# Performance work log

Hardware: AMD Instinct MI355X
Metric: run time of the kernel (lower is better)

The kernel has to match this reference:

```python
import jax, jax.numpy as jnp
import numpy as np

E = 1024
H = 16
D = E // H
T = 1024
S = 1024
B = 8
MASK_FILL = 1e-30  # note: module fills masked scores with 1e-30, NOT -inf


def setup_inputs() -> dict:
    key = jax.random.key(0)
    ks = jax.random.split(key, 8)
    inp = {
        "query1": jax.random.normal(ks[0], (T, B, E), jnp.float32),
        "query2": jax.random.normal(ks[1], (T, B, E), jnp.float32),
        "key": jax.random.normal(ks[2], (S, B, E), jnp.float32),
        "value": jax.random.normal(ks[3], (S, B, E), jnp.float32),
        # causal mask: True = masked
        "attn_mask": jnp.triu(jnp.ones((T, S), jnp.bool_), k=1),
        # xavier-uniform-ish weights (torch stores Linear weight as [out, in])
        "q_w": jax.random.uniform(ks[4], (E, E), jnp.float32, -1, 1) * np.sqrt(6.0 / (2 * E)),
        "k_w": jax.random.uniform(ks[5], (E, E), jnp.float32, -1, 1) * np.sqrt(6.0 / (2 * E)),
        "v_w": jax.random.uniform(ks[6], (E, E), jnp.float32, -1, 1) * np.sqrt(6.0 / (2 * E)),
        "out_w": jax.random.uniform(ks[7], (E, E), jnp.float32, -1, 1) * np.sqrt(6.0 / (2 * E)),
    }
    return inp


def _split_heads(x):
    # [L, B, E] -> [B, H, L, D]
    L = x.shape[0]
    return x.reshape(L, B, H, D).transpose(1, 2, 0, 3)


def reference(query1, query2, key, value, attn_mask, q_w, k_w, v_w, out_w):
    scaling = float(D) ** -0.5
    q1 = _split_heads(query1 @ q_w.T) * scaling  # [B,H,T,D]
    q2 = _split_heads(query2 @ q_w.T) * scaling
    k = _split_heads(key @ k_w.T)                # [B,H,S,D]
    v = _split_heads(value @ v_w.T)

    # ---- stream s (second query stream attends first) ----
    scores_s = jnp.einsum("bhtd,bhsd->bhts", q2, k)
    scores_s = jnp.where(attn_mask[None, None], MASK_FILL, scores_s)
    probs_s = jax.nn.softmax(scores_s, axis=-1)
    o_s = jnp.einsum("bhts,bhsd->bhtd", probs_s, v)  # [B,H,T,D]

    # k/v update between passes (requires T == S)
    k2 = k + o_s
    v2 = v + o_s

    # ---- stream d ----
    scores_d = jnp.einsum("bhtd,bhsd->bhts", q1, k2)
    scores_d = jnp.where(attn_mask[None, None], MASK_FILL, scores_d)
    probs_d = jax.nn.softmax(scores_d, axis=-1)
    o_d = jnp.einsum("bhts,bhsd->bhtd", probs_d, v2)

    def _merge_and_proj(o):
        # [B,H,T,D] -> [T,B,E] -> out proj (no bias)
        return o.transpose(2, 0, 1, 3).reshape(T, B, E) @ out_w.T

    attn_output_s = _merge_and_proj(o_s)
    attn_output_d = _merge_and_proj(o_d)
    attn_s = probs_s.mean(axis=1)  # [B,T,S]
    attn_d = probs_d.mean(axis=1)
    return attn_output_d, attn_d, attn_output_s, attn_s
```

## Files before the change

kernel.cpp:

```cpp
#include <hip/hip_runtime.h>
#include <cstddef>

#define T_DIM 1024
#define S_DIM 1024
#define B_DIM 8
#define E_DIM 1024
#define H_DIM 16
#define D_DIM 64
#define NBHTD (B_DIM*H_DIM*T_DIM*D_DIM)

typedef __attribute__((ext_vector_type(8))) short short8;
typedef __attribute__((ext_vector_type(4))) float floatx4;

__device__ inline unsigned short f2bf(float x){
    union { float f; unsigned u; } v; v.f = x;
    unsigned r = (v.u + 0x7FFFu + ((v.u >> 16) & 1u)) >> 16;
    return (unsigned short)r;
}
__device__ inline float bf2f(unsigned short h){
    union { float f; unsigned u; } v; v.u = ((unsigned)h) << 16; return v.f;
}

typedef __attribute__((address_space(1))) const unsigned int* gptr_t;
typedef __attribute__((address_space(3))) unsigned int* lptr_t;
__device__ inline void gl_lds16(const void* g, void* l){
    __builtin_amdgcn_global_load_lds((gptr_t)g, (lptr_t)l, 16, 0, 0);
}

__device__ inline int swz(int row, int s){
    int ch = (s >> 2) ^ (row & 7);
    return (row << 10) + (ch << 2) + (s & 3);
}

__global__ __launch_bounds__(256)
void split_pair(const float* __restrict__ src, unsigned short* __restrict__ hi,
                unsigned short* __restrict__ lo, float scale)
{
    size_t i = ((size_t)blockIdx.x*256 + threadIdx.x)*8;
    float4 a = *(const float4*)(src+i);
    float4 b = *(const float4*)(src+i+4);
    float v[8] = {a.x,a.y,a.z,a.w,b.x,b.y,b.z,b.w};
    short8 h8, l8;
    #pragma unroll
    for (int j = 0; j < 8; ++j) {
        float x = v[j]*scale;
        unsigned short hh = f2bf(x);
        h8[j] = (short)hh;
        l8[j] = (short)f2bf(x - bf2f(hh));
    }
    *(short8*)(hi+i) = h8;
    *(short8*)(lo+i) = l8;
}

template <int AMODE, int CMODE>
__global__ __launch_bounds__(256, 2)
void gemm_bf3(const unsigned short* __restrict__ Ahi, const unsigned short* __restrict__ Alo,
              const unsigned short* __restrict__ Bhi, const unsigned short* __restrict__ Blo,
              float* __restrict__ Cf,
              unsigned short* __restrict__ Chi, unsigned short* __restrict__ Clo)
{
    __shared__ __align__(16) unsigned short lds[4][128*32];

    const int tid  = threadIdx.x;
    const int n0   = blockIdx.x * 128;
    const int m0   = blockIdx.y * 128;
    const int wave = tid >> 6, lane = tid & 63;
    const int lrow = lane & 15, quad = lane >> 4;
    const int mw = (wave & 1)*64, nw = (wave >> 1)*64;

    floatx4 acc[4][4];
    #pragma unroll
    for (int i = 0; i < 4; ++i)
        #pragma unroll
        for (int j = 0; j < 4; ++j) acc[i][j] = (floatx4){0.f,0.f,0.f,0.f};

    for (int kk = 0; kk < 1024; kk += 32) {
        __syncthreads();
        #pragma unroll
        for (int rnd = 0; rnd < 2; ++rnd) {
            int c = rnd*256 + tid;
            int row = c >> 2, col8 = (c & 3)*8;
            size_t aoff;
            if (AMODE == 0) {
                aoff = (size_t)(m0+row)*1024 + kk + col8;
            } else {
                int r = m0 + row; int t = r >> 3, bb = r & 7;
                int h = kk >> 6, d0 = (kk & 63) + col8;
                aoff = (((size_t)(bb*H_DIM + h)*T_DIM) + t)*D_DIM + d0;
            }
            size_t boff = (size_t)(n0+row)*1024 + kk + col8;
            gl_lds16(Ahi + aoff, &lds[0][c*8]);
            gl_lds16(Alo + aoff, &lds[1][c*8]);
            gl_lds16(Bhi + boff, &lds[2][c*8]);
            gl_lds16(Blo + boff, &lds[3][c*8]);
        }
        __syncthreads();

        short8 ah[4], al[4], bh[4], bl[4];
        #pragma unroll
        for (int mt = 0; mt < 4; ++mt) {
            int r = mw + mt*16 + lrow;
            ah[mt] = *(const short8*)&lds[0][r*32 + quad*8];
            al[mt] = *(const short8*)&lds[1][r*32 + quad*8];
        }
        #pragma unroll
        for (int nt = 0; nt < 4; ++nt) {
            int r = nw + nt*16 + lrow;
            bh[nt] = *(const short8*)&lds[2][r*32 + quad*8];
            bl[nt] = *(const short8*)&lds[3][r*32 + quad*8];
        }
        #pragma unroll
        for (int mt = 0; mt < 4; ++mt)
            #pragma unroll
            for (int nt = 0; nt < 4; ++nt) {
                acc[mt][nt] = __builtin_amdgcn_mfma_f32_16x16x32_bf16(ah[mt], bh[nt], acc[mt][nt], 0,0,0);
                acc[mt][nt] = __builtin_amdgcn_mfma_f32_16x16x32_bf16(ah[mt], bl[nt], acc[mt][nt], 0,0,0);
                acc[mt][nt] = __builtin_amdgcn_mfma_f32_16x16x32_bf16(al[mt], bh[nt], acc[mt][nt], 0,0,0);
            }
    }

    #pragma unroll
    for (int mt = 0; mt < 4; ++mt) {
        #pragma unroll
        for (int nt = 0; nt < 4; ++nt) {
            int n = n0 + nw + nt*16 + lrow;
            #pragma unroll
            for (int r = 0; r < 4; ++r) {
                int m = m0 + mw + mt*16 + quad*4 + r;
                float v = acc[mt][nt][r];
                if (CMODE == 2) {
                    Cf[(size_t)m*1024 + n] = v;
                } else {
                    int t = m >> 3, bb = m & 7;
                    int h = n >> 6, d = n & 63;
                    size_t idx = (((size_t)(bb*H_DIM + h)*T_DIM) + t)*D_DIM + d;
                    if (CMODE == 0) {
                        Cf[idx] = v;
                    } else {
                        unsigned short hh = f2bf(v);
                        Chi[idx] = hh;
                        Clo[idx] = f2bf(v - bf2f(hh));
                    }
                }
            }
        }
    }
}

__global__ __launch_bounds__(256)
void split_vt(const float* __restrict__ Vh, unsigned short* __restrict__ Vthi,
              unsigned short* __restrict__ Vtlo)
{
    __shared__ float tile[64][68];
    const int bh = blockIdx.y, s0 = blockIdx.x*64;
    const int tid = threadIdx.x;
    const size_t base = (size_t)bh*S_DIM*D_DIM;

    {
        int r = tid >> 2, c0 = (tid & 3) * 16;
        const float* p = Vh + base + (size_t)(s0 + r)*D_DIM + c0;
        float4 a = *(const float4*)p;
        float4 b = *(const float4*)(p+4);
        float4 c = *(const float4*)(p+8);
        float4 d = *(const float4*)(p+12);
        *(float4*)&tile[r][c0]    = a;
        *(float4*)&tile[r][c0+4]  = b;
        *(float4*)&tile[r][c0+8]  = c;
        *(float4*)&tile[r][c0+12] = d;
    }
    __syncthreads();
    {
        int d = tid >> 2, cs = (tid & 3) * 16;
        short8 hi[2], lo[2];
        #pragma unroll
        for (int half = 0; half < 2; ++half)
            #pragma unroll
            for (int u = 0; u < 8; ++u) {
                float x = tile[cs + half*8 + u][d];
                unsigned short hh = f2bf(x);
                hi[half][u] = (short)hh;
                lo[half][u] = (short)f2bf(x - bf2f(hh));
            }
        size_t obase = base + (size_t)d*S_DIM + s0 + cs;
        *(short8*)(Vthi + obase)     = hi[0];
        *(short8*)(Vthi + obase + 8) = hi[1];
        *(short8*)(Vtlo + obase)     = lo[0];
        *(short8*)(Vtlo + obase + 8) = lo[1];
    }
}

__global__ __launch_bounds__(256, 2)
void attn_mfma(const float* __restrict__ Qh,
               const unsigned short* __restrict__ Khi, const unsigned short* __restrict__ Klo,
               const unsigned short* __restrict__ Vthi, const unsigned short* __restrict__ Vtlo,
               float* __restrict__ Ofp,
               unsigned short* __restrict__ Ohi, unsigned short* __restrict__ Olo,
               float* __restrict__ attn_mean)
{
    const int b  = blockIdx.y;
    const int t0 = blockIdx.x * 16;
    const int tid  = threadIdx.x;
    const int lane = tid & 63;
    const int wave = tid >> 6;
    const int lrow = lane & 15;
    const int quad = lane >> 4;

    __shared__ float sc[16 * 1024];

    float accm[4][16];
    #pragma unroll
    for (int j = 0; j < 4; ++j)
        #pragma unroll
        for (int c = 0; c < 16; ++c) accm[j][c] = 0.f;

    #pragma unroll 1
    for (int h = 0; h < H_DIM; ++h) {
        const int bh = b*H_DIM + h;
        const size_t kbase = (size_t)bh * S_DIM * D_DIM;

        short8 qh0, ql0, qh1, ql1;
        {
            const float* qp = Qh + kbase + (size_t)(t0 + lrow)*D_DIM + quad*8;
            float4 a  = *(const float4*)qp;
            float4 b4 = *(const float4*)(qp+4);
            float4 c4 = *(const float4*)(qp+32);
            float4 d4 = *(const float4*)(qp+36);
            float va[8] = {a.x,a.y,a.z,a.w,b4.x,b4.y,b4.z,b4.w};
            float vb8[8] = {c4.x,c4.y,c4.z,c4.w,d4.x,d4.y,d4.z,d4.w};
            #pragma unroll
            for (int j = 0; j < 8; ++j) {
                unsigned short h0 = f2bf(va[j]);
                qh0[j] = (short)h0; ql0[j] = (short)f2bf(va[j] - bf2f(h0));
                unsigned short h1 = f2bf(vb8[j]);
                qh1[j] = (short)h1; ql1[j] = (short)f2bf(vb8[j] - bf2f(h1));
            }
        }

        __syncthreads();

        #pragma unroll 1
        for (int jt = 0; jt < 16; ++jt) {
            const int s0 = wave*256 + jt*16;
            const unsigned short* kp_h = Khi + kbase + (size_t)(s0 + lrow)*D_DIM + quad*8;
            const unsigned short* kp_l = Klo + kbase + (size_t)(s0 + lrow)*D_DIM + quad*8;
            short8 kh0 = *(const short8*)(kp_h);
            short8 kh1 = *(const short8*)(kp_h + 32);
            short8 kl0 = *(const short8*)(kp_l);
            short8 kl1 = *(const short8*)(kp_l + 32);
            floatx4 acc = {0.f,0.f,0.f,0.f};
            acc = __builtin_amdgcn_mfma_f32_16x16x32_bf16(qh0, kh0, acc, 0,0,0);
            acc = __builtin_amdgcn_mfma_f32_16x16x32_bf16(qh1, kh1, acc, 0,0,0);
            acc = __builtin_amdgcn_mfma_f32_16x16x32_bf16(qh0, kl0, acc, 0,0,0);
            acc = __builtin_amdgcn_mfma_f32_16x16x32_bf16(qh1, kl1, acc, 0,0,0);
            acc = __builtin_amdgcn_mfma_f32_16x16x32_bf16(ql0, kh0, acc, 0,0,0);
            acc = __builtin_amdgcn_mfma_f32_16x16x32_bf16(ql1, kh1, acc, 0,0,0);
            const int s_g = s0 + lrow;
            #pragma unroll
            for (int r = 0; r < 4; ++r) {
                int q = quad*4 + r;
                float v = (s_g > t0 + q) ? 1e-30f : acc[r];
                sc[swz(q, s_g)] = v;
            }
        }
        __syncthreads();

        #pragma unroll 1
        for (int j = 0; j < 4; ++j) {
            const int row = wave*4 + j;
            float2 vb[8];
            float m = -3.0e38f;
            #pragma unroll
            for (int c = 0; c < 8; ++c) {
                int s = lane*2 + 128*c;
                vb[c] = *(const float2*)&sc[swz(row, s)];
                m = fmaxf(m, fmaxf(vb[c].x, vb[c].y));
            }
            #pragma unroll
            for (int off = 32; off > 0; off >>= 1) m = fmaxf(m, __shfl_xor(m, off));
            float sum = 0.f;
            #pragma unroll
            for (int c = 0; c < 8; ++c) {
                vb[c].x = __expf(vb[c].x - m);
                vb[c].y = __expf(vb[c].y - m);
                sum += vb[c].x + vb[c].y;
            }
            #pragma unroll
            for (int off = 32; off > 0; off >>= 1) sum += __shfl_xor(sum, off);
            const float inv = 1.0f / sum;
            #pragma unroll
            for (int c = 0; c < 8; ++c) {
                int s = lane*2 + 128*c;
                float p0 = vb[c].x * inv, p1 = vb[c].y * inv;
                accm[j][2*c]   += p0;
                accm[j][2*c+1] += p1;
                float2 pw; pw.x = p0; pw.y = p1;
                *(float2*)&sc[swz(row, s)] = pw;
            }
        }
        __syncthreads();

        {
            const int d0 = wave*16;
            const unsigned short* vh = Vthi + kbase + (size_t)(d0 + lrow)*S_DIM;
            const unsigned short* vl = Vtlo + kbase + (size_t)(d0 + lrow)*S_DIM;
            floatx4 oa = {0.f,0.f,0.f,0.f}, ob = {0.f,0.f,0.f,0.f};
            #pragma unroll 2
            for (int sk = 0; sk < S_DIM; sk += 32) {
                const int sa = sk + quad*8;
                float4 p0 = *(const float4*)&sc[swz(lrow, sa)];
                float4 p1 = *(const float4*)&sc[swz(lrow, sa+4)];
                short8 af;
                af[0]=(short)f2bf(p0.x); af[1]=(short)f2bf(p0.y);
                af[2]=(short)f2bf(p0.z); af[3]=(short)f2bf(p0.w);
                af[4]=(short)f2bf(p1.x); af[5]=(short)f2bf(p1.y);
                af[6]=(short)f2bf(p1.z); af[7]=(short)f2bf(p1.w);
                short8 bh8 = *(const short8*)(vh + sa);
                short8 bl8 = *(const short8*)(vl + sa);
                oa = __builtin_amdgcn_mfma_f32_16x16x32_bf16(af, bh8, oa, 0,0,0);
                ob = __builtin_amdgcn_mfma_f32_16x16x32_bf16(af, bl8, ob, 0,0,0);
            }
            #pragma unroll
            for (int r = 0; r < 4; ++r) {
                int q = quad*4 + r;
                float v = oa[r] + ob[r];
                size_t idx = kbase + (size_t)(t0+q)*D_DIM + d0 + lrow;
                if (Ofp) Ofp[idx] = v;
                unsigned short hh = f2bf(v);
                Ohi[idx] = hh;
                Olo[idx] = f2bf(v - bf2f(hh));
            }
        }
    }

    #pragma unroll
    for (int j = 0; j < 4; ++j) {
        int row = wave*4 + j;
        #pragma unroll
        for (int c = 0; c < 8; ++c) {
            float2 p;
            p.x = accm[j][2*c]   * (1.0f/H_DIM);
            p.y = accm[j][2*c+1] * (1.0f/H_DIM);
            *(float2*)&attn_mean[((size_t)b*T_DIM + t0 + row)*S_DIM + lane*2 + 128*c] = p;
        }
    }
}

__global__ __launch_bounds__(256)
void add_k(unsigned short* __restrict__ Khi, unsigned short* __restrict__ Klo,
           const float* __restrict__ O)
{
    size_t i = ((size_t)blockIdx.x*256 + threadIdx.x)*8;
    short8 hi = *(short8*)(Khi+i), lo = *(short8*)(Klo+i);
    float4 o0 = *(const float4*)(O+i), o1 = *(const float4*)(O+i+4);
    float ov[8] = {o0.x,o0.y,o0.z,o0.w,o1.x,o1.y,o1.z,o1.w};
    short8 nh, nl;
    #pragma unroll
    for (int j = 0; j < 8; ++j) {
        float k = bf2f((unsigned short)hi[j]) + bf2f((unsigned short)lo[j]) + ov[j];
        unsigned short hh = f2bf(k);
        nh[j] = (short)hh;
        nl[j] = (short)f2bf(k - bf2f(hh));
    }
    *(short8*)(Khi+i) = nh;
    *(short8*)(Klo+i) = nl;
}

__global__ __launch_bounds__(256)
void add_v(float* __restrict__ V, const float* __restrict__ O)
{
    size_t i = ((size_t)blockIdx.x*256 + threadIdx.x)*4;
    float4 o = *(const float4*)(O+i);
    float4 v = *(const float4*)(V+i);
    v.x+=o.x; v.y+=o.y; v.z+=o.z; v.w+=o.w;
    *(float4*)(V+i) = v;
}

extern "C" void kernel_launch(void* const* d_in, const int* in_sizes, int n_in,
                              void* d_out, int out_size, void* d_ws, size_t ws_size,
                              hipStream_t stream)
{
    const float* q1  = (const float*)d_in[0];
    const float* q2  = (const float*)d_in[1];
    const float* key = (const float*)d_in[2];
    const float* val = (const float*)d_in[3];
    const float* qw  = (const float*)d_in[5];
    const float* kw  = (const float*)d_in[6];
    const float* vw  = (const float*)d_in[7];
    const float* ow  = (const float*)d_in[8];

    float* out   = (float*)d_out;
    float* outd  = out;
    float* attnd = out + 1*(size_t)NBHTD;
    float* outs  = out + 2*(size_t)NBHTD;
    float* attns = out + 3*(size_t)NBHTD;

    unsigned short* ws_u16 = (unsigned short*)d_ws;
    unsigned short* Khi  = ws_u16;
    unsigned short* Klo  = Khi  + (size_t)NBHTD;
    unsigned short* Vthi = Klo  + (size_t)NBHTD;
    unsigned short* Vtlo = Vthi + (size_t)NBHTD;
    unsigned short* R2a  = Vtlo + (size_t)NBHTD;
    unsigned short* R2b  = R2a  + 2*(size_t)NBHTD;

    const size_t EE = (size_t)E_DIM*E_DIM;
    unsigned short* qwhi = R2a;
    unsigned short* qwlo = qwhi + EE;
    unsigned short* kwhi = qwlo + EE;
    unsigned short* kwlo = kwhi + EE;
    unsigned short* vwhi = kwlo + EE;
    unsigned short* vwlo = vwhi + EE;
    float* Osb = (float*)R2a;
    unsigned short* Odhi = R2a;
    unsigned short* Odlo = Odhi + (size_t)NBHTD;
    unsigned short* Oshi = R2b;
    unsigned short* Oslo = Oshi + (size_t)NBHTD;
    unsigned short* owhi = ws_u16;
    unsigned short* owlo = owhi + EE;

    float* Q1h = outd;
    float* Q2h = outs;
    float* Vh  = attnd;
    unsigned short* Ahi = (unsigned short*)attns;
    unsigned short* Alo = Ahi + (size_t)NBHTD;

    const dim3 ggrid(8, 64);

    split_pair<<<512, 256, 0, stream>>>(qw, qwhi, qwlo, 1.f);
    split_pair<<<512, 256, 0, stream>>>(kw, kwhi, kwlo, 1.f);
    split_pair<<<512, 256, 0, stream>>>(vw, vwhi, vwlo, 1.f);

    split_pair<<<4096, 256, 0, stream>>>(key, Ahi, Alo, 1.f);
    gemm_bf3<0,1><<<ggrid, 256, 0, stream>>>(Ahi, Alo, kwhi, kwlo, nullptr, Khi, Klo);

    split_pair<<<4096, 256, 0, stream>>>(val, Ahi, Alo, 1.f);
    gemm_bf3<0,0><<<ggrid, 256, 0, stream>>>(Ahi, Alo, vwhi, vwlo, Vh, nullptr, nullptr);
    split_vt<<<dim3(16, 128), 256, 0, stream>>>(Vh, Vthi, Vtlo);

    split_pair<<<4096, 256, 0, stream>>>(q1, Ahi, Alo, 0.125f);
    gemm_bf3<0,0><<<ggrid, 256, 0, stream>>>(Ahi, Alo, qwhi, qwlo, Q1h, nullptr, nullptr);

    split_pair<<<4096, 256, 0, stream>>>(q2, Ahi, Alo, 0.125f);
    gemm_bf3<0,0><<<ggrid, 256, 0, stream>>>(Ahi, Alo, qwhi, qwlo, Q2h, nullptr, nullptr);

    attn_mfma<<<dim3(64, 8), 256, 0, stream>>>(Q2h, Khi, Klo, Vthi, Vtlo,
                                               Osb, Oshi, Oslo, attns);

    add_k<<<4096, 256, 0, stream>>>(Khi, Klo, Osb);
    add_v<<<8192, 256, 0, stream>>>(Vh, Osb);
    split_vt<<<dim3(16, 128), 256, 0, stream>>>(Vh, Vthi, Vtlo);

    attn_mfma<<<dim3(64, 8), 256, 0, stream>>>(Q1h, Khi, Klo, Vthi, Vtlo,
                                               nullptr, Odhi, Odlo, attnd);

    split_pair<<<512, 256, 0, stream>>>(ow, owhi, owlo, 1.f);
    gemm_bf3<1,2><<<ggrid, 256, 0, stream>>>(Oshi, Oslo, owhi, owlo, outs, nullptr, nullptr);
    gemm_bf3<1,2><<<ggrid, 256, 0, stream>>>(Odhi, Odlo, owhi, owlo, outd, nullptr, nullptr);
}
```

Baseline: 1.895 ms.

## Keep attention scores in registers with split softmax and bf16 P in LDS

The attention kernel now swaps the MFMA operand order so each lane holds a column of scores in registers. Softmax runs in registers, and only per-wave max and sum pairs are exchanged through LDS, instead of writing fp32 scores to LDS and reading them back. Probabilities are converted to bf16 once and stored in a smaller swizzled LDS buffer, which the PV stage reads directly. The change also software-prefetches K tiles, remaps the grid so adjacent blocks span batches, and widens the attn_mean stores to float4. The cost is much higher register pressure (sv, accm, mt arrays), which may cause spills or lower occupancy.

```diff
diff --git a/kernel.cpp b/kernel.cpp
--- a/kernel.cpp
+++ b/kernel.cpp
@@ -10,6 +10,7 @@
 #define NBHTD (B_DIM*H_DIM*T_DIM*D_DIM)
 
 typedef __attribute__((ext_vector_type(8))) short short8;
+typedef __attribute__((ext_vector_type(4))) short short4v;
 typedef __attribute__((ext_vector_type(4))) float floatx4;
 
 __device__ inline unsigned short f2bf(float x){
@@ -27,9 +28,8 @@
     __builtin_amdgcn_global_load_lds((gptr_t)g, (lptr_t)l, 16, 0, 0);
 }
 
-__device__ inline int swz(int row, int s){
-    int ch = (s >> 2) ^ (row & 7);
-    return (row << 10) + (ch << 2) + (s & 3);
+__device__ inline int poff(int row, int s){
+    return (row << 10) + ((((s >> 3) ^ (row & 7)) << 3)) + (s & 7);
 }
 
 __global__ __launch_bounds__(256)
@@ -197,21 +197,22 @@
                unsigned short* __restrict__ Ohi, unsigned short* __restrict__ Olo,
                float* __restrict__ attn_mean)
 {
-    const int b  = blockIdx.y;
-    const int t0 = blockIdx.x * 16;
+    const int bid = blockIdx.x;
+    const int b   = bid & 7;
+    const int t0  = (bid >> 3) * 16;
     const int tid  = threadIdx.x;
     const int lane = tid & 63;
     const int wave = tid >> 6;
     const int lrow = lane & 15;
     const int quad = lane >> 4;
-
-    __shared__ float sc[16 * 1024];
-
-    float accm[4][16];
+    const int t_g  = t0 + lrow;
+
+    __shared__ __align__(16) unsigned short plds[16*1024];
+    __shared__ float2 stats[4][16];
+
+    float accm[64];
     #pragma unroll
-    for (int j = 0; j < 4; ++j)
-        #pragma unroll
-        for (int c = 0; c < 16; ++c) accm[j][c] = 0.f;
+    for (int i = 0; i < 64; ++i) accm[i] = 0.f;
 
     #pragma unroll 1
     for (int h = 0; h < H_DIM; ++h) {
@@ -225,7 +226,7 @@
             float4 b4 = *(const float4*)(qp+4);
             float4 c4 = *(const float4*)(qp+32);
             float4 d4 = *(const float4*)(qp+36);
-            float va[8] = {a.x,a.y,a.z,a.w,b4.x,b4.y,b4.z,b4.w};
+            float va[8]  = {a.x,a.y,a.z,a.w,b4.x,b4.y,b4.z,b4.w};
             float vb8[8] = {c4.x,c4.y,c4.z,c4.w,d4.x,d4.y,d4.z,d4.w};
             #pragma unroll
             for (int j = 0; j < 8; ++j) {
@@ -236,66 +237,85 @@
             }
         }
 
+        float sv[64];
+        {
+            const unsigned short* kph = Khi + kbase + (size_t)(wave*256 + lrow)*D_DIM + quad*8;
+            const unsigned short* kpl = Klo + kbase + (size_t)(wave*256 + lrow)*D_DIM + quad*8;
+            short8 kh0 = *(const short8*)(kph);
+            short8 kh1 = *(const short8*)(kph + 32);
+            short8 kl0 = *(const short8*)(kpl);
+            short8 kl1 = *(const short8*)(kpl + 32);
+            #pragma unroll
+            for (int jt = 0; jt < 16; ++jt) {
+                short8 nh0, nh1, nl0, nl1;
+                if (jt < 15) {
+                    const unsigned short* nph = kph + (jt+1)*16*D_DIM;
+                    const unsigned short* npl = kpl + (jt+1)*16*D_DIM;
+                    nh0 = *(const short8*)(nph);
+                    nh1 = *(const short8*)(nph + 32);
+                    nl0 = *(const short8*)(npl);
+                    nl1 = *(const short8*)(npl + 32);
+                }
+                floatx4 acc = {0.f,0.f,0.f,0.f};
+                acc = __builtin_amdgcn_mfma_f32_16x16x32_bf16(kh0, qh0, acc, 0,0,0);
+                acc = __builtin_amdgcn_mfma_f32_16x16x32_bf16(kh1, qh1, acc, 0,0,0);
+                acc = __builtin_amdgcn_mfma_f32_16x16x32_bf16(kl0, qh0, acc, 0,0,0);
+                acc = __builtin_amdgcn_mfma_f32_16x16x32_bf16(kl1, qh1, acc, 0,0,0);
+                acc = __builtin_amdgcn_mfma_f32_16x16x32_bf16(kh0, ql0, acc, 0,0,0);
+                acc = __builtin_amdgcn_mfma_f32_16x16x32_bf16(kh1, ql1, acc, 0,0,0);
+                const int sb = wave*256 + jt*16 + quad*4;
+                #pragma unroll
+                for (int r = 0; r < 4; ++r)
+                    sv[jt*4+r] = (sb + r > t_g) ? 1e-30f : acc[r];
+                kh0 = nh0; kh1 = nh1; kl0 = nl0; kl1 = nl1;
+            }
+        }
+
+        float mt[32];
+        #pragma unroll
+        for (int i = 0; i < 32; ++i) mt[i] = fmaxf(sv[i], sv[i+32]);
+        #pragma unroll
+        for (int st = 16; st > 0; st >>= 1) {
+            #pragma unroll
+            for (int i = 0; i < st; ++i) mt[i] = fmaxf(mt[i], mt[i+st]);
+        }
+        float m_loc = fmaxf(mt[0], __shfl_xor(mt[0], 16));
+        m_loc = fmaxf(m_loc, __shfl_xor(m_loc, 32));
+
+        #pragma unroll
+        for (int i = 0; i < 64; ++i) sv[i] = __expf(sv[i] - m_loc);
+        float st2[32];
+        #pragma unroll
+        for (int i = 0; i < 32; ++i) st2[i] = sv[i] + sv[i+32];
+        #pragma unroll
+        for (int st = 16; st > 0; st >>= 1) {
+            #pragma unroll
+            for (int i = 0; i < st; ++i) st2[i] += st2[i+st];
+        }
+        float s_loc = st2[0] + __shfl_xor(st2[0], 16);
+        s_loc += __shfl_xor(s_loc, 32);
+
+        if (quad == 0) stats[wave][lrow] = make_float2(m_loc, s_loc);
         __syncthreads();
 
-        #pragma unroll 1
+        float2 c0 = stats[0][lrow], c1 = stats[1][lrow];
+        float2 c2 = stats[2][lrow], c3 = stats[3][lrow];
+        float m_g = fmaxf(fmaxf(c0.x, c1.x), fmaxf(c2.x, c3.x));
+        float sum_g = c0.y*__expf(c0.x - m_g) + c1.y*__expf(c1.x - m_g)
+                    + c2.y*__expf(c2.x - m_g) + c3.y*__expf(c3.x - m_g);
+        const float myscale = __expf(m_loc - m_g) / sum_g;
+
+        #pragma unroll
         for (int jt = 0; jt < 16; ++jt) {
-            const int s0 = wave*256 + jt*16;
-            const unsigned short* kp_h = Khi + kbase + (size_t)(s0 + lrow)*D_DIM + quad*8;
-            const unsigned short* kp_l = Klo + kbase + (size_t)(s0 + lrow)*D_DIM + quad*8;
-            short8 kh0 = *(const short8*)(kp_h);
-            short8 kh1 = *(const short8*)(kp_h + 32);
-            short8 kl0 = *(const short8*)(kp_l);
-            short8 kl1 = *(const short8*)(kp_l + 32);
-            floatx4 acc = {0.f,0.f,0.f,0.f};
-            acc = __builtin_amdgcn_mfma_f32_16x16x32_bf16(qh0, kh0, acc, 0,0,0);
-            acc = __builtin_amdgcn_mfma_f32_16x16x32_bf16(qh1, kh1, acc, 0,0,0);
-            acc = __builtin_amdgcn_mfma_f32_16x16x32_bf16(qh0, kl0, acc, 0,0,0);
-            acc = __builtin_amdgcn_mfma_f32_16x16x32_bf16(qh1, kl1, acc, 0,0,0);
-            acc = __builtin_amdgcn_mfma_f32_16x16x32_bf16(ql0, kh0, acc, 0,0,0);
-            acc = __builtin_amdgcn_mfma_f32_16x16x32_bf16(ql1, kh1, acc, 0,0,0);
-            const int s_g = s0 + lrow;
-            #pragma unroll
-            for (int r = 0; r < 4; ++r) {
-                int q = quad*4 + r;
-                float v = (s_g > t0 + q) ? 1e-30f : acc[r];
-                sc[swz(q, s_g)] = v;
-            }
-        }
-        __syncthreads();
-
-        #pragma unroll 1
-        for (int j = 0; j < 4; ++j) {
-            const int row = wave*4 + j;
-            float2 vb[8];
-            float m = -3.0e38f;
-            #pragma unroll
-            for (int c = 0; c < 8; ++c) {
-                int s = lane*2 + 128*c;
-                vb[c] = *(const float2*)&sc[swz(row, s)];
-                m = fmaxf(m, fmaxf(vb[c].x, vb[c].y));
-            }
-            #pragma unroll
-            for (int off = 32; off > 0; off >>= 1) m = fmaxf(m, __shfl_xor(m, off));
-            float sum = 0.f;
-            #pragma unroll
-            for (int c = 0; c < 8; ++c) {
-                vb[c].x = __expf(vb[c].x - m);
-                vb[c].y = __expf(vb[c].y - m);
-                sum += vb[c].x + vb[c].y;
-            }
-            #pragma unroll
-            for (int off = 32; off > 0; off >>= 1) sum += __shfl_xor(sum, off);
-            const float inv = 1.0f / sum;
-            #pragma unroll
-            for (int c = 0; c < 8; ++c) {
-                int s = lane*2 + 128*c;
-                float p0 = vb[c].x * inv, p1 = vb[c].y * inv;
-                accm[j][2*c]   += p0;
-                accm[j][2*c+1] += p1;
-                float2 pw; pw.x = p0; pw.y = p1;
-                *(float2*)&sc[swz(row, s)] = pw;
-            }
+            float p0 = sv[jt*4+0]*myscale, p1 = sv[jt*4+1]*myscale;
+            float p2 = sv[jt*4+2]*myscale, p3 = sv[jt*4+3]*myscale;
+            accm[jt*4+0] += p0; accm[jt*4+1] += p1;
+            accm[jt*4+2] += p2; accm[jt*4+3] += p3;
+            short4v pk;
+            pk[0] = (short)f2bf(p0); pk[1] = (short)f2bf(p1);
+            pk[2] = (short)f2bf(p2); pk[3] = (short)f2bf(p3);
+            const int sidx = wave*256 + jt*16 + quad*4;
+            *(short4v*)&plds[poff(lrow, sidx)] = pk;
         }
         __syncthreads();
 
@@ -304,16 +324,10 @@
             const unsigned short* vh = Vthi + kbase + (size_t)(d0 + lrow)*S_DIM;
             const unsigned short* vl = Vtlo + kbase + (size_t)(d0 + lrow)*S_DIM;
             floatx4 oa = {0.f,0.f,0.f,0.f}, ob = {0.f,0.f,0.f,0.f};
-            #pragma unroll 2
+            #pragma unroll 4
             for (int sk = 0; sk < S_DIM; sk += 32) {
                 const int sa = sk + quad*8;
-                float4 p0 = *(const float4*)&sc[swz(lrow, sa)];
-                float4 p1 = *(const float4*)&sc[swz(lrow, sa+4)];
-                short8 af;
-                af[0]=(short)f2bf(p0.x); af[1]=(short)f2bf(p0.y);
-                af[2]=(short)f2bf(p0.z); af[3]=(short)f2bf(p0.w);
-                af[4]=(short)f2bf(p1.x); af[5]=(short)f2bf(p1.y);
-                af[6]=(short)f2bf(p1.z); af[7]=(short)f2bf(p1.w);
+                short8 af  = *(const short8*)&plds[poff(lrow, sa)];
                 short8 bh8 = *(const short8*)(vh + sa);
                 short8 bl8 = *(const short8*)(vl + sa);
                 oa = __builtin_amdgcn_mfma_f32_16x16x32_bf16(af, bh8, oa, 0,0,0);
@@ -332,15 +346,16 @@
         }
     }
 
-    #pragma unroll
-    for (int j = 0; j < 4; ++j) {
-        int row = wave*4 + j;
-        #pragma unroll
-        for (int c = 0; c < 8; ++c) {
-            float2 p;
-            p.x = accm[j][2*c]   * (1.0f/H_DIM);
-            p.y = accm[j][2*c+1] * (1.0f/H_DIM);
-            *(float2*)&attn_mean[((size_t)b*T_DIM + t0 + row)*S_DIM + lane*2 + 128*c] = p;
+    {
+        float* am = attn_mean + ((size_t)b*T_DIM + t_g)*S_DIM + wave*256 + quad*4;
+        #pragma unroll
+        for (int jt = 0; jt < 16; ++jt) {
+            float4 p4;
+            p4.x = accm[jt*4+0]*(1.0f/H_DIM);
+            p4.y = accm[jt*4+1]*(1.0f/H_DIM);
+            p4.z = accm[jt*4+2]*(1.0f/H_DIM);
+            p4.w = accm[jt*4+3]*(1.0f/H_DIM);
+            *(float4*)(am + jt*16) = p4;
         }
     }
 }
@@ -442,15 +457,15 @@
     split_pair<<<4096, 256, 0, stream>>>(q2, Ahi, Alo, 0.125f);
     gemm_bf3<0,0><<<ggrid, 256, 0, stream>>>(Ahi, Alo, qwhi, qwlo, Q2h, nullptr, nullptr);
 
-    attn_mfma<<<dim3(64, 8), 256, 0, stream>>>(Q2h, Khi, Klo, Vthi, Vtlo,
-                                               Osb, Oshi, Oslo, attns);
+    attn_mfma<<<dim3(512), 256, 0, stream>>>(Q2h, Khi, Klo, Vthi, Vtlo,
+                                             Osb, Oshi, Oslo, attns);
 
     add_k<<<4096, 256, 0, stream>>>(Khi, Klo, Osb);
     add_v<<<8192, 256, 0, stream>>>(Vh, Osb);
     split_vt<<<dim3(16, 128), 256, 0, stream>>>(Vh, Vthi, Vtlo);
 
-    attn_mfma<<<dim3(64, 8), 256, 0, stream>>>(Q1h, Khi, Klo, Vthi, Vtlo,
-                                               nullptr, Odhi, Odlo, attnd);
+    attn_mfma<<<dim3(512), 256, 0, stream>>>(Q1h, Khi, Klo, Vthi, Vtlo,
+                                             nullptr, Odhi, Odlo, attnd);
 
     split_pair<<<512, 256, 0, stream>>>(ow, owhi, owlo, 1.f);
     gemm_bf3<1,2><<<ggrid, 256, 0, stream>>>(Oshi, Oslo, owhi, owlo, outs, nullptr, nullptr);
```

Result: faster. 1.625 ms (-14.2%).
